# Kernel optimization log

Hardware: AMD Instinct MI355X
Metric: run time of the kernel (lower is better)

## Reference

```python
import jax, jax.numpy as jnp
import numpy as np

B, T, C = 2, 2048, 2048
N_HEADS, N_KV_HEADS = 16, 4
HEAD_DIM = C // N_HEADS  # 128
NUM_GROUPS = N_HEADS // N_KV_HEADS  # 4


def setup_inputs() -> dict:
    key = jax.random.key(0)
    ks = jax.random.split(key, 5)
    s = 1.0 / np.sqrt(C)
    return {
        "x": jax.random.normal(ks[0], (B, T, C), dtype=jnp.float32),
        "Wq": jax.random.normal(ks[1], (C, N_HEADS * HEAD_DIM), dtype=jnp.float32) * s,
        "Wk": jax.random.normal(ks[2], (C, N_KV_HEADS * HEAD_DIM), dtype=jnp.float32) * s,
        "Wv": jax.random.normal(ks[3], (C, N_KV_HEADS * HEAD_DIM), dtype=jnp.float32) * s,
        "Wo": jax.random.normal(ks[4], (C, C), dtype=jnp.float32) * s,
    }


def _rope_tables(seq_len, head_dim, dtype):
    theta = 1.0 / (10000.0 ** (jnp.arange(0, head_dim, 2, dtype=jnp.float32) / head_dim))
    freqs = jnp.arange(seq_len, dtype=jnp.float32)[:, None] * theta[None, :]  # [T, hd/2]
    cos = jnp.concatenate([jnp.cos(freqs), jnp.cos(freqs)], axis=-1)  # [T, hd]
    sin = jnp.concatenate([jnp.sin(freqs), jnp.sin(freqs)], axis=-1)
    return cos.astype(dtype), sin.astype(dtype)


def _rotate_half(x):
    x1, x2 = jnp.split(x, 2, axis=-1)
    return jnp.concatenate([-x2, x1], axis=-1)


def reference(x, Wq, Wk, Wv, Wo):
    b, t, c = x.shape
    q = (x @ Wq).reshape(b, t, N_HEADS, HEAD_DIM).transpose(0, 2, 1, 3)      # [B,H,T,hd]
    k = (x @ Wk).reshape(b, t, N_KV_HEADS, HEAD_DIM).transpose(0, 2, 1, 3)   # [B,Hkv,T,hd]
    v = (x @ Wv).reshape(b, t, N_KV_HEADS, HEAD_DIM).transpose(0, 2, 1, 3)

    cos, sin = _rope_tables(t, HEAD_DIM, x.dtype)  # [T,hd]
    cos = cos[None, None]  # [1,1,T,hd]
    sin = sin[None, None]
    q = q * cos + _rotate_half(q) * sin
    k = k * cos + _rotate_half(k) * sin

    # GQA: expand kv heads (repeat_interleave along head dim)
    k = jnp.repeat(k, NUM_GROUPS, axis=1)  # [B,H,T,hd]
    v = jnp.repeat(v, NUM_GROUPS, axis=1)

    scale = 1.0 / jnp.sqrt(jnp.asarray(HEAD_DIM, dtype=x.dtype))
    scores = jnp.einsum("bhqd,bhkd->bhqk", q, k) * scale  # [B,H,T,T]
    causal = jnp.tril(jnp.ones((t, t), dtype=bool))
    scores = jnp.where(causal[None, None], scores, jnp.asarray(-jnp.inf, dtype=scores.dtype))
    attn = jax.nn.softmax(scores, axis=-1)
    out = jnp.einsum("bhqk,bhkd->bhqd", attn, v)  # [B,H,T,hd]
    out = out.transpose(0, 2, 1, 3).reshape(b, t, c)
    return out @ Wo
```

## Files before the change

### kernel.cpp

```cpp
#include <hip/hip_runtime.h>
#include <hip/hip_bf16.h>
#include <math.h>

typedef __hip_bfloat16 bf16;
typedef __attribute__((ext_vector_type(8))) short bf16x8;
typedef __attribute__((ext_vector_type(4))) float floatx4;

__device__ __forceinline__ void async_copy16(const bf16* g, bf16* l) {
    __builtin_amdgcn_global_load_lds(
        (__attribute__((address_space(1))) void*)(void*)g,
        (__attribute__((address_space(3))) void*)(void*)l,
        16, 0, 0);
}

__global__ __launch_bounds__(256) void cast_f32_bf16(const float* __restrict__ in,
                                                     bf16* __restrict__ out, int n4) {
    int i = blockIdx.x * 256 + threadIdx.x;
    if (i >= n4) return;
    float4 v = ((const float4*)in)[i];
    union { ushort4 u; bf16 b[4]; } o;
    o.b[0] = __float2bfloat16(v.x);
    o.b[1] = __float2bfloat16(v.y);
    o.b[2] = __float2bfloat16(v.z);
    o.b[3] = __float2bfloat16(v.w);
    ((ushort4*)out)[i] = o.u;
}

__global__ __launch_bounds__(256) void cast_transpose(const float* __restrict__ in,
                                                      bf16* __restrict__ out, int K, int N) {
    __shared__ float tile[32][33];
    int nb = blockIdx.x * 32, kb = blockIdx.y * 32;
    for (int j = threadIdx.y; j < 32; j += 8)
        tile[j][threadIdx.x] = in[(size_t)(kb + j) * N + nb + threadIdx.x];
    __syncthreads();
    for (int j = threadIdx.y; j < 32; j += 8)
        out[(size_t)(nb + j) * K + kb + threadIdx.x] = __float2bfloat16(tile[threadIdx.x][j]);
}

template <bool OUTF32>
__global__ __launch_bounds__(256) void gemm_bt(const bf16* __restrict__ A,
                                               const bf16* __restrict__ Bt,
                                               void* __restrict__ Cout,
                                               int M, int N, int K) {
    __shared__ bf16 As[128 * 32];
    __shared__ bf16 Bs[128 * 32];
    const int tid = threadIdx.x;
    const int wave = tid >> 6, lane = tid & 63;
    const int c = lane & 15, quad = lane >> 4;
    const int wm = wave >> 1, wn = wave & 1;
    const int mBase = blockIdx.y * 128, nBase = blockIdx.x * 128;

    const int sRow = lane >> 2;
    const int sCol = ((lane & 3) ^ ((lane >> 3) & 3)) << 3;
    const int rdOff = (quad ^ ((c >> 1) & 3)) << 3;
    const bf16* gA = A + (size_t)(mBase + wave * 32 + sRow) * K + sCol;
    const bf16* gB = Bt + (size_t)(nBase + wave * 32 + sRow) * K + sCol;
    bf16* lA = As + wave * 1024;
    bf16* lB = Bs + wave * 1024;

    floatx4 acc[4][4];
#pragma unroll
    for (int mt = 0; mt < 4; mt++)
#pragma unroll
        for (int nt = 0; nt < 4; nt++) acc[mt][nt] = (floatx4){0.f, 0.f, 0.f, 0.f};

    for (int k0 = 0; k0 < K; k0 += 32) {
        async_copy16(gA + k0, lA);
        async_copy16(gA + k0 + 16 * K, lA + 512);
        async_copy16(gB + k0, lB);
        async_copy16(gB + k0 + 16 * K, lB + 512);
        __syncthreads();
        bf16x8 af[4], bfr[4];
#pragma unroll
        for (int mt = 0; mt < 4; mt++)
            af[mt] = *(const bf16x8*)(As + (wm * 64 + mt * 16 + c) * 32 + rdOff);
#pragma unroll
        for (int nt = 0; nt < 4; nt++)
            bfr[nt] = *(const bf16x8*)(Bs + (wn * 64 + nt * 16 + c) * 32 + rdOff);
#pragma unroll
        for (int mt = 0; mt < 4; mt++)
#pragma unroll
            for (int nt = 0; nt < 4; nt++)
                acc[mt][nt] = __builtin_amdgcn_mfma_f32_16x16x32_bf16(af[mt], bfr[nt],
                                                                      acc[mt][nt], 0, 0, 0);
        __syncthreads();
    }
#pragma unroll
    for (int mt = 0; mt < 4; mt++)
#pragma unroll
        for (int nt = 0; nt < 4; nt++)
#pragma unroll
            for (int r = 0; r < 4; r++) {
                int row = mBase + wm * 64 + mt * 16 + quad * 4 + r;
                int col = nBase + wn * 64 + nt * 16 + c;
                if (OUTF32)
                    ((float*)Cout)[(size_t)row * N + col] = acc[mt][nt][r];
                else
                    ((bf16*)Cout)[(size_t)row * N + col] = __float2bfloat16(acc[mt][nt][r]);
            }
}

__global__ __launch_bounds__(256) void rope_kernel(bf16* __restrict__ X, int heads, int rowStride) {
    int idx = blockIdx.x * 256 + threadIdx.x;
    int d = idx & 63;
    int h = (idx >> 6) % heads;
    int row = idx / (heads * 64);
    int t = row & 2047;
    float theta = exp2f(-(float)d * 0.20762050593045827f);
    float ang = (float)t * theta;
    float sv, cv;
    __sincosf(ang, &sv, &cv);
    bf16* p = X + (size_t)row * rowStride + h * 128 + d;
    float x1 = __bfloat162float(p[0]);
    float x2 = __bfloat162float(p[64]);
    p[0]  = __float2bfloat16(x1 * cv - x2 * sv);
    p[64] = __float2bfloat16(x2 * cv + x1 * sv);
}

__global__ __launch_bounds__(256) void vtrans(const bf16* __restrict__ QKV,
                                              bf16* __restrict__ Vtg) {
    __shared__ bf16 tile[32][34];
    const int bh = blockIdx.z;
    const int b = bh >> 2, kvh = bh & 3;
    const int t0 = blockIdx.x * 32, d0 = blockIdx.y * 32;
    const bf16* src = QKV + (size_t)b * 2048 * 3072 + 2560 + kvh * 128;
    for (int j = threadIdx.y; j < 32; j += 8)
        tile[j][threadIdx.x] = src[(size_t)(t0 + j) * 3072 + d0 + threadIdx.x];
    __syncthreads();
    bf16* dst = Vtg + (size_t)bh * 128 * 2048;
    for (int j = threadIdx.y; j < 32; j += 8)
        dst[(size_t)(d0 + j) * 2048 + t0 + threadIdx.x] = tile[threadIdx.x][j];
}

__global__ __launch_bounds__(256, 4) void flash_attn5(const bf16* __restrict__ QKV,
                                                      const bf16* __restrict__ Vtg,
                                                      bf16* __restrict__ Slot0,
                                                      bf16* __restrict__ Slot1,
                                                      float* __restrict__ Ls) {
    const int T = 2048, STR = 3072;
    __shared__ bf16 Ks[4 * 64 * 32];
    __shared__ bf16 Vs[2 * 128 * 32];
    __shared__ bf16 Pl[4][16 * 40];
    const int b = blockIdx.z, h = blockIdx.y;
    const int pj = blockIdx.x >> 1, s = blockIdx.x & 1;
    const int kvh = h >> 2;
    const int tid = threadIdx.x, wave = tid >> 6, lane = tid & 63;
    const int c = lane & 15, quad = lane >> 4;
    const float C2 = 0.12751541717525597f;

    const bf16* Kg = QKV + (size_t)b * T * STR + 2048 + kvh * 128;
    const bf16* Vg = Vtg + (size_t)(b * 4 + kvh) * 128 * 2048;
    const int srow = tid >> 2;
    const int xcol = ((tid & 3) ^ ((tid >> 3) & 3)) << 3;
    const int koff = (quad ^ ((c >> 1) & 3)) << 3;
    bf16* PlW = &Pl[wave][0];
    const int qa = 31 - pj;

    auto run_part = [&](int qtile, int ktlo, int kthi, bf16* slot, int lsSlot) {
        const int q0 = qtile * 64;
        bf16x8 qf[4];
        {
            const bf16* qp = QKV + ((size_t)b * T + q0 + wave * 16 + c) * STR + h * 128 + quad * 8;
#pragma unroll
            for (int ks = 0; ks < 4; ks++) qf[ks] = *(const bf16x8*)(qp + ks * 32);
            const float t = (float)(q0 + wave * 16 + c);
#pragma unroll
            for (int ks = 0; ks < 2; ks++)
#pragma unroll
                for (int j = 0; j < 8; j++) {
                    int d = ks * 32 + quad * 8 + j;
                    float theta = exp2f((float)d * -0.20762050593045827f);
                    float sv, cv;
                    __sincosf(t * theta, &sv, &cv);
                    float lo = __bfloat162float(((const bf16*)&qf[ks])[j]);
                    float hi = __bfloat162float(((const bf16*)&qf[ks + 2])[j]);
                    ((bf16*)&qf[ks])[j]     = __float2bfloat16((lo * cv - hi * sv) * C2);
                    ((bf16*)&qf[ks + 2])[j] = __float2bfloat16((hi * cv + lo * sv) * C2);
                }
        }
        floatx4 accO[8];
#pragma unroll
        for (int nt = 0; nt < 8; nt++) accO[nt] = (floatx4){0.f, 0.f, 0.f, 0.f};
        float lrow[4] = {0.f, 0.f, 0.f, 0.f};

        for (int kt = ktlo; kt < kthi; kt++) {
            const int kt0 = kt * 64;
#pragma unroll
            for (int it = 0; it < 4; it++) {
                async_copy16(Kg + (size_t)(kt0 + srow) * STR + it * 32 + xcol,
                             Ks + it * 2048 + wave * 512);
                async_copy16(Vg + (size_t)((it & 1) * 64 + srow) * 2048 + kt0 + (it >> 1) * 32 + xcol,
                             Vs + it * 2048 + wave * 512);
            }
            __syncthreads();
            floatx4 sf[4];
#pragma unroll
            for (int nt = 0; nt < 4; nt++) sf[nt] = (floatx4){0.f, 0.f, 0.f, 0.f};
#pragma unroll
            for (int ks = 0; ks < 4; ks++)
#pragma unroll
                for (int nt = 0; nt < 4; nt++) {
                    bf16x8 kf = *(const bf16x8*)(Ks + ks * 2048 + (nt * 16 + c) * 32 + koff);
                    sf[nt] = __builtin_amdgcn_mfma_f32_16x16x32_bf16(qf[ks], kf, sf[nt], 0, 0, 0);
                }
            const int lim = (kt == qtile) ? (wave * 16 + quad * 4) : 1000;
#pragma unroll
            for (int kc = 0; kc < 2; kc++) {
#pragma unroll
                for (int nt2 = 0; nt2 < 2; nt2++) {
                    const int nt = kc * 2 + nt2;
#pragma unroll
                    for (int r = 0; r < 4; r++) {
                        float p = exp2f(sf[nt][r]);
                        if (nt * 16 + c > lim + r) p = 0.f;
                        lrow[r] += p;
                        PlW[(quad * 4 + r) * 40 + nt2 * 16 + c] = __float2bfloat16(p);
                    }
                }
                asm volatile("s_waitcnt lgkmcnt(0)" ::: "memory");
                bf16x8 pf = *(const bf16x8*)(PlW + c * 40 + quad * 8);
#pragma unroll
                for (int nt = 0; nt < 8; nt++) {
                    bf16x8 vf = *(const bf16x8*)(Vs + kc * 4096 + (nt * 16 + c) * 32 + koff);
                    accO[nt] = __builtin_amdgcn_mfma_f32_16x16x32_bf16(pf, vf, accO[nt], 0, 0, 0);
                }
                asm volatile("" ::: "memory");
            }
            __syncthreads();
        }
        float sred[4];
#pragma unroll
        for (int r = 0; r < 4; r++) {
            float v = lrow[r];
            v += __shfl_xor(v, 1);
            v += __shfl_xor(v, 2);
            v += __shfl_xor(v, 4);
            v += __shfl_xor(v, 8);
            sred[r] = v;
        }
        if (c == 0) {
#pragma unroll
            for (int r = 0; r < 4; r++)
                Ls[(size_t)lsSlot * 65536 + ((size_t)(b * 16 + h) * 32 + qtile) * 64
                   + wave * 16 + quad * 4 + r] = sred[r];
        }
        const size_t orow = (size_t)b * T + q0 + wave * 16 + quad * 4;
#pragma unroll
        for (int nt = 0; nt < 8; nt++)
#pragma unroll
            for (int r = 0; r < 4; r++)
                slot[(orow + r) * 2048 + h * 128 + nt * 16 + c] =
                    __float2bfloat16(accO[nt][r]);
    };

    if (s == 0) {
        run_part(qa, 0, 17, Slot0, 0);
    } else {
        run_part(qa, 17, 32 - pj, Slot1, 1);
        run_part(pj, 0, pj + 1, Slot0, 0);
    }
}

__global__ __launch_bounds__(256) void attn_merge(bf16* __restrict__ AO,
                                                  const bf16* __restrict__ P1,
                                                  const float* __restrict__ Ls) {
    int i = blockIdx.x * 256 + threadIdx.x;
    int row = i >> 8;
    int cg = (i & 255) << 3;
    int b = row >> 11, t = row & 2047;
    int qtile = t >> 6;
    int h = cg >> 7;
    size_t off = (size_t)row * 2048 + cg;
    size_t li = ((size_t)(b * 16 + h) * 32 + qtile) * 64 + (t & 63);
    bf16x8 a0 = *(const bf16x8*)(AO + off);
    float l = Ls[li];
    float acc[8];
#pragma unroll
    for (int j = 0; j < 8; j++) acc[j] = __bfloat162float(((const bf16*)&a0)[j]);
    if (qtile >= 16) {
        bf16x8 a1 = *(const bf16x8*)(P1 + off);
        l += Ls[65536 + li];
#pragma unroll
        for (int j = 0; j < 8; j++) acc[j] += __bfloat162float(((const bf16*)&a1)[j]);
    }
    float inv = 1.0f / l;
    bf16x8 o;
#pragma unroll
    for (int j = 0; j < 8; j++) ((bf16*)&o)[j] = __float2bfloat16(acc[j] * inv);
    *(bf16x8*)(AO + off) = o;
}

extern "C" void kernel_launch(void* const* d_in, const int* in_sizes, int n_in,
                              void* d_out, int out_size, void* d_ws, size_t ws_size,
                              hipStream_t stream) {
    const float* x  = (const float*)d_in[0];
    const float* Wq = (const float*)d_in[1];
    const float* Wk = (const float*)d_in[2];
    const float* Wv = (const float*)d_in[3];
    const float* Wo = (const float*)d_in[4];

    char* ws = (char*)d_ws;
    bf16* xb   = (bf16*)(ws);
    bf16* Vtg  = (bf16*)(ws);
    bf16* Slt1 = (bf16*)(ws + 4194304);
    float* Ls  = (float*)(ws + 20971520);
    bf16* Wt   = (bf16*)(ws + 16777216);
    bf16* Wot  = (bf16*)(ws + 29360128);
    bf16* QKV  = (bf16*)(ws + 37748736);
    bf16* AO   = (bf16*)(ws + 62914560);

    cast_f32_bf16<<<8192, 256, 0, stream>>>(x, xb, 2097152);
    cast_transpose<<<dim3(64, 64), dim3(32, 8), 0, stream>>>(Wq, Wt, 2048, 2048);
    cast_transpose<<<dim3(16, 64), dim3(32, 8), 0, stream>>>(Wk, Wt + 2048 * 2048, 2048, 512);
    cast_transpose<<<dim3(16, 64), dim3(32, 8), 0, stream>>>(Wv, Wt + 2560 * 2048, 2048, 512);
    cast_transpose<<<dim3(64, 64), dim3(32, 8), 0, stream>>>(Wo, Wot, 2048, 2048);

    gemm_bt<false><<<dim3(24, 32), 256, 0, stream>>>(xb, Wt, QKV, 4096, 3072, 2048);

    rope_kernel<<<4096, 256, 0, stream>>>(QKV + 2048, 4, 3072);

    vtrans<<<dim3(64, 4, 8), dim3(32, 8), 0, stream>>>(QKV, Vtg);

    flash_attn5<<<dim3(32, 16, 2), 256, 0, stream>>>(QKV, Vtg, AO, Slt1, Ls);

    attn_merge<<<4096, 256, 0, stream>>>(AO, Slt1, Ls);

    gemm_bt<true><<<dim3(16, 32), 256, 0, stream>>>(AO, Wot, d_out, 4096, 2048, 2048);
}
```

Baseline: 324.1 us.

## Use 256x256-tile 512-thread GEMM with 4-stage async LDS pipeline for QKV projection

Adds a new GEMM kernel with 256x256 output tiles, 8 waves, a 4-buffer LDS ring filled via global_load_lds two tiles ahead, XOR-swizzled LDS layout and s_setprio around MFMA blocks. It replaces the 128x128 GEMM for the QKV projection to raise arithmetic intensity and overlap loads with compute. The grid shrinks to 192 blocks, which is fewer than the CU count and may underfill the GPU. Register pressure also rises from 128 accumulators per thread.

```diff
diff --git a/kernel.cpp b/kernel.cpp
--- a/kernel.cpp
+++ b/kernel.cpp
@@ -97,6 +97,103 @@
                     ((float*)Cout)[(size_t)row * N + col] = acc[mt][nt][r];
                 else
                     ((bf16*)Cout)[(size_t)row * N + col] = __float2bfloat16(acc[mt][nt][r]);
+            }
+}
+
+__global__ __launch_bounds__(512) void gemm256(const bf16* __restrict__ A,
+                                               const bf16* __restrict__ Bt,
+                                               bf16* __restrict__ C,
+                                               int M, int N, int K) {
+    __shared__ bf16 As[4][256 * 32];
+    __shared__ bf16 Bs[4][256 * 32];
+    const int tid = threadIdx.x;
+    const int wave = tid >> 6, lane = tid & 63;
+    const int c = lane & 15, quad = lane >> 4;
+    const int wm = wave >> 2, wn = wave & 3;
+    const int mBase = blockIdx.y * 256, nBase = blockIdx.x * 256;
+    const int rdOff = (quad ^ ((c >> 1) & 3)) << 3;
+
+    const bf16* gAs[2];
+    const bf16* gBs[2];
+#pragma unroll
+    for (int i = 0; i < 2; i++) {
+        int ci = i * 512 + tid;
+        int r = ci >> 2;
+        int sc = (ci & 3) ^ ((r >> 1) & 3);
+        gAs[i] = A + (size_t)(mBase + r) * K + sc * 8;
+        gBs[i] = Bt + (size_t)(nBase + r) * K + sc * 8;
+    }
+    const int ldsW = wave * 512;
+
+    floatx4 acc[8][4];
+#pragma unroll
+    for (int mt = 0; mt < 8; mt++)
+#pragma unroll
+        for (int nt = 0; nt < 4; nt++) acc[mt][nt] = (floatx4){0.f, 0.f, 0.f, 0.f};
+
+    auto stage_half = [&](int t, int i) {
+        const int bb = t & 3;
+        const int lo = i * 4096 + ldsW;
+        async_copy16(gAs[i] + (size_t)t * 32, &As[bb][0] + lo);
+        async_copy16(gBs[i] + (size_t)t * 32, &Bs[bb][0] + lo);
+    };
+
+    auto tile_body = [&](int t, bool doStage) {
+        const int bb = t & 3;
+        const bf16* as = &As[bb][0];
+        const bf16* bs = &Bs[bb][0];
+        bf16x8 bfr[4], af[4];
+#pragma unroll
+        for (int nt = 0; nt < 4; nt++)
+            bfr[nt] = *(const bf16x8*)(bs + (wn * 64 + nt * 16 + c) * 32 + rdOff);
+#pragma unroll
+        for (int mt = 0; mt < 4; mt++)
+            af[mt] = *(const bf16x8*)(as + (wm * 128 + mt * 16 + c) * 32 + rdOff);
+        if (doStage) stage_half(t + 2, 0);
+        __builtin_amdgcn_s_setprio(1);
+#pragma unroll
+        for (int mt = 0; mt < 4; mt++)
+#pragma unroll
+            for (int nt = 0; nt < 4; nt++)
+                acc[mt][nt] = __builtin_amdgcn_mfma_f32_16x16x32_bf16(af[mt], bfr[nt],
+                                                                      acc[mt][nt], 0, 0, 0);
+        __builtin_amdgcn_s_setprio(0);
+#pragma unroll
+        for (int mt = 0; mt < 4; mt++)
+            af[mt] = *(const bf16x8*)(as + (wm * 128 + 64 + mt * 16 + c) * 32 + rdOff);
+        if (doStage) stage_half(t + 2, 1);
+        __builtin_amdgcn_s_setprio(1);
+#pragma unroll
+        for (int mt = 0; mt < 4; mt++)
+#pragma unroll
+            for (int nt = 0; nt < 4; nt++)
+                acc[4 + mt][nt] = __builtin_amdgcn_mfma_f32_16x16x32_bf16(af[mt], bfr[nt],
+                                                                          acc[4 + mt][nt], 0, 0, 0);
+        __builtin_amdgcn_s_setprio(0);
+    };
+
+    const int NT = K >> 5;
+    stage_half(0, 0); stage_half(0, 1);
+    stage_half(1, 0); stage_half(1, 1);
+    asm volatile("s_waitcnt vmcnt(4)\n\ts_barrier" ::: "memory");
+
+    for (int t = 0; t < NT - 2; ++t) {
+        tile_body(t, true);
+        asm volatile("s_waitcnt vmcnt(4)\n\ts_barrier" ::: "memory");
+    }
+    tile_body(NT - 2, false);
+    asm volatile("s_waitcnt vmcnt(0)\n\ts_barrier" ::: "memory");
+    tile_body(NT - 1, false);
+
+#pragma unroll
+    for (int mt = 0; mt < 8; mt++)
+#pragma unroll
+        for (int nt = 0; nt < 4; nt++)
+#pragma unroll
+            for (int r = 0; r < 4; r++) {
+                int row = mBase + wm * 128 + mt * 16 + quad * 4 + r;
+                int col = nBase + wn * 64 + nt * 16 + c;
+                C[(size_t)row * N + col] = __float2bfloat16(acc[mt][nt][r]);
             }
 }
 
@@ -315,7 +412,7 @@
     cast_transpose<<<dim3(16, 64), dim3(32, 8), 0, stream>>>(Wv, Wt + 2560 * 2048, 2048, 512);
     cast_transpose<<<dim3(64, 64), dim3(32, 8), 0, stream>>>(Wo, Wot, 2048, 2048);
 
-    gemm_bt<false><<<dim3(24, 32), 256, 0, stream>>>(xb, Wt, QKV, 4096, 3072, 2048);
+    gemm256<<<dim3(12, 16), 512, 0, stream>>>(xb, Wt, QKV, 4096, 3072, 2048);
 
     rope_kernel<<<4096, 256, 0, stream>>>(QKV + 2048, 4, 3072);
 
```

Measured after the change: 314.6 us. 1.03x faster.
